# Performance work log

Hardware: AMD Instinct MI355X
Metric: run time of the kernel (lower is better)

## Reference

```python
import jax, jax.numpy as jnp
import numpy as np

N_NODES = 50000
N_EDGES = 800000
HIDDEN = 128


def setup_inputs() -> dict:
    key = jax.random.key(0)
    k_emb, k_ei, k1, k2, k3, kb1, kb2, kb3 = jax.random.split(key, 8)
    emb = jax.random.normal(k_emb, (N_NODES, HIDDEN), dtype=jnp.float32)
    edge_index = jax.random.randint(k_ei, (2, N_EDGES), 0, N_NODES, dtype=jnp.int64)
    h = HIDDEN
    # MLP([2h, 4h, h, 1]) weights, Kaiming-uniform-ish init
    def lin(k, fan_in, fan_out):
        bound = 1.0 / np.sqrt(fan_in)
        return jax.random.uniform(k, (fan_in, fan_out), jnp.float32, -bound, bound)
    W1 = lin(k1, 2 * h, 4 * h)
    b1 = jax.random.uniform(kb1, (4 * h,), jnp.float32, -1.0 / np.sqrt(2 * h), 1.0 / np.sqrt(2 * h))
    W2 = lin(k2, 4 * h, h)
    b2 = jax.random.uniform(kb2, (h,), jnp.float32, -1.0 / np.sqrt(4 * h), 1.0 / np.sqrt(4 * h))
    W3 = lin(k3, h, 1)
    b3 = jax.random.uniform(kb3, (1,), jnp.float32, -1.0 / np.sqrt(h), 1.0 / np.sqrt(h))
    return {"emb": emb, "edge_index": edge_index,
            "W1": W1, "b1": b1, "W2": W2, "b2": b2, "W3": W3, "b3": b3}


def reference(emb, edge_index, W1, b1, W2, b2, W3, b3):
    # learn_edge_att=True path: gather endpoints, concat, 3-layer MLP
    col, row = edge_index[0], edge_index[1]
    f12 = jnp.concatenate([emb[col], emb[row]], axis=-1)  # [E, 2h]
    x = jax.nn.relu(f12 @ W1 + b1)                         # [E, 4h]
    x = jax.nn.relu(x @ W2 + b2)                           # [E, h]
    att_log_logits = x @ W3 + b3                           # [E, 1]
    return att_log_logits
```

## Files before the change

### kernel.cpp

```cpp
#include <hip/hip_runtime.h>
#include <hip/hip_bf16.h>
#include <stdint.h>

#define N_EDGES   800000
#define N_NODESC  50000
#define HID       128

typedef __attribute__((ext_vector_type(8))) short bf16x8;
typedef __attribute__((ext_vector_type(4))) float f32x4;
typedef __attribute__((ext_vector_type(4))) unsigned int u32x4;

__device__ __forceinline__ short f2bf(float f) {
    union { float f; uint32_t u; } v; v.f = f;
    uint32_t r = v.u + 0x7FFFu + ((v.u >> 16) & 1u);
    return (short)(r >> 16);
}

__device__ __forceinline__ uint32_t packbf2(float lo, float hi) {
    float2 t; t.x = lo; t.y = hi;
    __hip_bfloat162 h = __float22bfloat162_rn(t);
    uint32_t u;
    __builtin_memcpy(&u, &h, 4);
    return u;
}

__device__ __forceinline__ uint32_t addrelu2(uint32_t a, uint32_t b) {
    __hip_bfloat162 ha, hb;
    __builtin_memcpy(&ha, &a, 4);
    __builtin_memcpy(&hb, &b, 4);
    __hip_bfloat162 s = __hadd2(ha, hb);
    uint32_t x;
    __builtin_memcpy(&x, &s, 4);
    uint32_t neg = (x & 0x80008000u) >> 15;
    return x & ~(neg * 0xFFFFu);
}
__device__ __forceinline__ bf16x8 addrelu8(u32x4 p, u32x4 q) {
    u32x4 r;
    #pragma unroll
    for (int j = 0; j < 4; ++j) r[j] = addrelu2(p[j], q[j]);
    bf16x8 out;
    __builtin_memcpy(&out, &r, 16);
    return out;
}

#define PQ_OFF   0UL
#define W1S_OFF  102400000UL
#define W2S_OFF  (W1S_OFF + 262144UL)

__global__ __launch_bounds__(256) void swizzle_kernel(const float* __restrict__ W1,
                                                      const float* __restrict__ W2,
                                                      short* __restrict__ W1s,
                                                      short* __restrict__ W2s) {
    int t = blockIdx.x * 256 + threadIdx.x;
    int lane = t & 63;
    int kq = lane >> 4;
    int nn = lane & 15;
    if (t < 16384) {
        int frag = t >> 6;
        int kc = frag >> 6;
        int nt = frag & 63;
        int n = nt * 16 + nn;
        int kbase = kc * 32 + kq * 8;
        bf16x8 v;
        #pragma unroll
        for (int j = 0; j < 8; ++j) {
            int k = kbase + j;
            float f = (n < 512) ? W1[k * 512 + n] : W1[(128 + k) * 512 + (n - 512)];
            v[j] = f2bf(f);
        }
        *(bf16x8*)(W1s + frag * 512 + lane * 8) = v;
    } else if (t < 24576) {
        int t2 = t - 16384;
        int frag = t2 >> 6;
        int kc = frag >> 3;
        int nt = frag & 7;
        int n = nt * 16 + nn;
        int kbase = kc * 32 + kq * 8;
        bf16x8 v;
        #pragma unroll
        for (int j = 0; j < 8; ++j) v[j] = f2bf(W2[(kbase + j) * HID + n]);
        *(bf16x8*)(W2s + frag * 512 + lane * 8) = v;
    }
}

__global__ __launch_bounds__(256) void precompute_kernel(const float* __restrict__ emb,
                                                         const short* __restrict__ W1s,
                                                         const float* __restrict__ b1,
                                                         short* __restrict__ PQ) {
    __shared__ short tile[4][16][272];
    int lane = threadIdx.x & 63;
    int w = threadIdx.x >> 6;
    int nb = blockIdx.x * 16;
    int m = lane & 15;
    int kq = lane >> 4;

    const float* arow = emb + (size_t)(nb + m) * 128 + kq * 8;

    f32x4 acc[16];
    #pragma unroll
    for (int i = 0; i < 16; ++i) acc[i] = (f32x4){0.f, 0.f, 0.f, 0.f};

    #pragma unroll
    for (int kc = 0; kc < 4; ++kc) {
        f32x4 x0 = *(const f32x4*)(arow + kc * 32);
        f32x4 x1 = *(const f32x4*)(arow + kc * 32 + 4);
        u32x4 au;
        au[0] = packbf2(x0[0], x0[1]); au[1] = packbf2(x0[2], x0[3]);
        au[2] = packbf2(x1[0], x1[1]); au[3] = packbf2(x1[2], x1[3]);
        bf16x8 a;
        __builtin_memcpy(&a, &au, 16);
        #pragma unroll
        for (int nt = 0; nt < 16; ++nt) {
            int frag = kc * 64 + (w * 16 + nt);
            bf16x8 b = *(const bf16x8*)(W1s + frag * 512 + lane * 8);
            acc[nt] = __builtin_amdgcn_mfma_f32_16x16x32_bf16(a, b, acc[nt], 0, 0, 0);
        }
    }

    #pragma unroll
    for (int nt = 0; nt < 16; ++nt) {
        int n = w * 256 + nt * 16 + m;
        float bias = (n < 512) ? b1[n] : 0.0f;
        #pragma unroll
        for (int r = 0; r < 4; ++r)
            tile[w][kq * 4 + r][nt * 16 + m] = f2bf(acc[nt][r] + bias);
    }

    #pragma unroll
    for (int s = 0; s < 8; ++s) {
        int row = s * 2 + (lane >> 5);
        int chunk = lane & 31;
        bf16x8 v = *(const bf16x8*)(&tile[w][row][chunk * 8]);
        *(bf16x8*)(PQ + (size_t)(nb + row) * 1024 + w * 256 + chunk * 8) = v;
    }
}

__global__ __launch_bounds__(256, 2) void edge_kernel(const short* __restrict__ PQ,
                                                      const int* __restrict__ ei,
                                                      const short* __restrict__ W2s,
                                                      const float* __restrict__ b2,
                                                      const float* __restrict__ W3,
                                                      const float* __restrict__ b3,
                                                      float* __restrict__ out) {
    int lane = threadIdx.x & 63;
    int w = threadIdx.x >> 6;
    int e0 = blockIdx.x * 256 + w * 64;
    int m = lane & 15;
    int kq = lane >> 4;

    int idx_c = ei[e0 + lane];
    int idx_r = ei[N_EDGES + e0 + lane];

    const short* pb[4];
    const short* qb[4];
    #pragma unroll
    for (int t = 0; t < 4; ++t) {
        int ce = __shfl(idx_c, t * 16 + m, 64);
        int re = __shfl(idx_r, t * 16 + m, 64);
        pb[t] = PQ + (size_t)ce * 1024 + kq * 8;
        qb[t] = PQ + (size_t)re * 1024 + 512 + kq * 8;
    }

    f32x4 acc[4][8];
    #pragma unroll
    for (int t = 0; t < 4; ++t)
        #pragma unroll
        for (int nt = 0; nt < 8; ++nt) acc[t][nt] = (f32x4){0.f, 0.f, 0.f, 0.f};

    #pragma unroll
    for (int kc = 0; kc < 16; ++kc) {
        u32x4 p[4], q[4];
        #pragma unroll
        for (int t = 0; t < 4; ++t) {
            p[t] = *(const u32x4*)(pb[t] + kc * 32);
            q[t] = *(const u32x4*)(qb[t] + kc * 32);
        }
        bf16x8 b[8];
        #pragma unroll
        for (int nt = 0; nt < 8; ++nt)
            b[nt] = *(const bf16x8*)(W2s + (kc * 8 + nt) * 512 + lane * 8);
        #pragma unroll
        for (int t = 0; t < 4; ++t) {
            bf16x8 a = addrelu8(p[t], q[t]);
            #pragma unroll
            for (int nt = 0; nt < 8; ++nt)
                acc[t][nt] = __builtin_amdgcn_mfma_f32_16x16x32_bf16(a, b[nt], acc[t][nt], 0, 0, 0);
        }
    }

    float b2v[8], w3v[8];
    #pragma unroll
    for (int nt = 0; nt < 8; ++nt) {
        b2v[nt] = b2[nt * 16 + m];
        w3v[nt] = W3[nt * 16 + m];
    }
    float b3s = b3[0];
    #pragma unroll
    for (int t = 0; t < 4; ++t) {
        float partial[4] = {0.f, 0.f, 0.f, 0.f};
        #pragma unroll
        for (int nt = 0; nt < 8; ++nt) {
            #pragma unroll
            for (int r = 0; r < 4; ++r) {
                float x2 = acc[t][nt][r] + b2v[nt];
                x2 = x2 > 0.f ? x2 : 0.f;
                partial[r] += x2 * w3v[nt];
            }
        }
        #pragma unroll
        for (int r = 0; r < 4; ++r) {
            #pragma unroll
            for (int off = 1; off < 16; off <<= 1)
                partial[r] += __shfl_xor(partial[r], off, 64);
            if (m == 0) out[e0 + t * 16 + kq * 4 + r] = partial[r] + b3s;
        }
    }
}

extern "C" void kernel_launch(void* const* d_in, const int* in_sizes, int n_in,
                              void* d_out, int out_size, void* d_ws, size_t ws_size,
                              hipStream_t stream) {
    const float* emb = (const float*)d_in[0];
    const int*   ei  = (const int*)d_in[1];
    const float* W1  = (const float*)d_in[2];
    const float* b1  = (const float*)d_in[3];
    const float* W2  = (const float*)d_in[4];
    const float* b2  = (const float*)d_in[5];
    const float* W3  = (const float*)d_in[6];
    const float* b3  = (const float*)d_in[7];
    float* out = (float*)d_out;

    short* PQ  = (short*)((char*)d_ws + PQ_OFF);
    short* W1s = (short*)((char*)d_ws + W1S_OFF);
    short* W2s = (short*)((char*)d_ws + W2S_OFF);

    swizzle_kernel<<<96, 256, 0, stream>>>(W1, W2, W1s, W2s);
    precompute_kernel<<<N_NODESC / 16, 256, 0, stream>>>(emb, W1s, b1, PQ);
    edge_kernel<<<N_EDGES / 256, 256, 0, stream>>>(PQ, ei, W2s, b2, W3, b3, out);
}
```

Measured before the change: 396.6 us.

## Counting-sort edges by source node to improve gather locality in edge kernel

Adds a histogram, prefix-scan and atomic scatter pipeline that reorders edges by their column index, storing sorted col/row and original edge ids. The edge kernel then reads the sorted indices, so edges sharing a source node reuse the same P row from cache, and it writes results back through the original ids. This trades several extra small kernel launches and atomic traffic for better locality on half of the random PQ gathers.

```diff
diff --git a/kernel.cpp b/kernel.cpp
--- a/kernel.cpp
+++ b/kernel.cpp
@@ -43,9 +43,17 @@
     return out;
 }
 
-#define PQ_OFF   0UL
-#define W1S_OFF  102400000UL
-#define W2S_OFF  (W1S_OFF + 262144UL)
+#define PQ_OFF    0UL
+#define W1S_OFF   102400000UL
+#define W2S_OFF   (W1S_OFF + 262144UL)
+#define CNT_OFF   (W2S_OFF + 131072UL)
+#define BSUM_OFF  (CNT_OFF + 200704UL)
+#define CUR_OFF   (BSUM_OFF + 1024UL)
+#define SCOL_OFF  (CUR_OFF + 200704UL)
+#define SROW_OFF  (SCOL_OFF + 3200000UL)
+#define SID_OFF   (SROW_OFF + 3200000UL)
+
+#define SCAN_BLOCKS 196
 
 __global__ __launch_bounds__(256) void swizzle_kernel(const float* __restrict__ W1,
                                                       const float* __restrict__ W2,
@@ -135,8 +143,73 @@
     }
 }
 
+
+__global__ __launch_bounds__(256) void zero_kernel(int* __restrict__ counts) {
+    counts[blockIdx.x * 256 + threadIdx.x] = 0;
+}
+
+__global__ __launch_bounds__(256) void hist_kernel(const int* __restrict__ ei,
+                                                   int* __restrict__ counts) {
+    int e = blockIdx.x * 256 + threadIdx.x;
+    atomicAdd(&counts[ei[e]], 1);
+}
+
+__global__ __launch_bounds__(256) void scan1_kernel(const int* __restrict__ counts,
+                                                    int* __restrict__ cursor,
+                                                    int* __restrict__ blocksum) {
+    __shared__ int sm[256];
+    int t = threadIdx.x;
+    int i = blockIdx.x * 256 + t;
+    int v = counts[i];
+    sm[t] = v;
+    __syncthreads();
+    #pragma unroll
+    for (int off = 1; off < 256; off <<= 1) {
+        int y = (t >= off) ? sm[t - off] : 0;
+        __syncthreads();
+        sm[t] += y;
+        __syncthreads();
+    }
+    cursor[i] = sm[t] - v;
+    if (t == 255) blocksum[blockIdx.x] = sm[t];
+}
+
+__global__ __launch_bounds__(256) void scan2_kernel(int* __restrict__ blocksum) {
+    __shared__ int sm[256];
+    int t = threadIdx.x;
+    sm[t] = (t < SCAN_BLOCKS) ? blocksum[t] : 0;
+    __syncthreads();
+    if (t == 0) {
+        int run = 0;
+        for (int i = 0; i < SCAN_BLOCKS; ++i) { int c = sm[i]; sm[i] = run; run += c; }
+    }
+    __syncthreads();
+    if (t < SCAN_BLOCKS) blocksum[t] = sm[t];
+}
+
+__global__ __launch_bounds__(256) void finalize_kernel(int* __restrict__ cursor,
+                                                       const int* __restrict__ blockbase) {
+    cursor[blockIdx.x * 256 + threadIdx.x] += blockbase[blockIdx.x];
+}
+
+__global__ __launch_bounds__(256) void scatter_kernel(const int* __restrict__ ei,
+                                                      int* __restrict__ cursor,
+                                                      int* __restrict__ scol,
+                                                      int* __restrict__ srow,
+                                                      int* __restrict__ sid) {
+    int e = blockIdx.x * 256 + threadIdx.x;
+    int c = ei[e];
+    int r = ei[N_EDGES + e];
+    int pos = atomicAdd(&cursor[c], 1);
+    scol[pos] = c;
+    srow[pos] = r;
+    sid[pos]  = e;
+}
+
 __global__ __launch_bounds__(256, 2) void edge_kernel(const short* __restrict__ PQ,
-                                                      const int* __restrict__ ei,
+                                                      const int* __restrict__ scol,
+                                                      const int* __restrict__ srow,
+                                                      const int* __restrict__ sid,
                                                       const short* __restrict__ W2s,
                                                       const float* __restrict__ b2,
                                                       const float* __restrict__ W3,
@@ -148,8 +221,9 @@
     int m = lane & 15;
     int kq = lane >> 4;
 
-    int idx_c = ei[e0 + lane];
-    int idx_r = ei[N_EDGES + e0 + lane];
+    int idx_c = scol[e0 + lane];
+    int idx_r = srow[e0 + lane];
+    int idx_o = sid[e0 + lane];
 
     const short* pb[4];
     const short* qb[4];
@@ -212,7 +286,8 @@
             #pragma unroll
             for (int off = 1; off < 16; off <<= 1)
                 partial[r] += __shfl_xor(partial[r], off, 64);
-            if (m == 0) out[e0 + t * 16 + kq * 4 + r] = partial[r] + b3s;
+            int oe = __shfl(idx_o, t * 16 + kq * 4 + r, 64);
+            if (m == 0) out[oe] = partial[r] + b3s;
         }
     }
 }
@@ -230,11 +305,24 @@
     const float* b3  = (const float*)d_in[7];
     float* out = (float*)d_out;
 
-    short* PQ  = (short*)((char*)d_ws + PQ_OFF);
-    short* W1s = (short*)((char*)d_ws + W1S_OFF);
-    short* W2s = (short*)((char*)d_ws + W2S_OFF);
+    short* PQ   = (short*)((char*)d_ws + PQ_OFF);
+    short* W1s  = (short*)((char*)d_ws + W1S_OFF);
+    short* W2s  = (short*)((char*)d_ws + W2S_OFF);
+    int* counts = (int*)((char*)d_ws + CNT_OFF);
+    int* bsum   = (int*)((char*)d_ws + BSUM_OFF);
+    int* cursor = (int*)((char*)d_ws + CUR_OFF);
+    int* scol   = (int*)((char*)d_ws + SCOL_OFF);
+    int* srow   = (int*)((char*)d_ws + SROW_OFF);
+    int* sid    = (int*)((char*)d_ws + SID_OFF);
 
     swizzle_kernel<<<96, 256, 0, stream>>>(W1, W2, W1s, W2s);
+    zero_kernel<<<SCAN_BLOCKS, 256, 0, stream>>>(counts);
+    hist_kernel<<<N_EDGES / 256, 256, 0, stream>>>(ei, counts);
+    scan1_kernel<<<SCAN_BLOCKS, 256, 0, stream>>>(counts, cursor, bsum);
+    scan2_kernel<<<1, 256, 0, stream>>>(bsum);
+    finalize_kernel<<<SCAN_BLOCKS, 256, 0, stream>>>(cursor, bsum);
+    scatter_kernel<<<N_EDGES / 256, 256, 0, stream>>>(ei, cursor, scol, srow, sid);
+
     precompute_kernel<<<N_NODESC / 16, 256, 0, stream>>>(emb, W1s, b1, PQ);
-    edge_kernel<<<N_EDGES / 256, 256, 0, stream>>>(PQ, ei, W2s, b2, W3, b3, out);
-}
+    edge_kernel<<<N_EDGES / 256, 256, 0, stream>>>(PQ, scol, srow, sid, W2s, b2, W3, b3, out);
+}
```

Measured after the change: 449.4 us. 1.13x slower.
